# Optimization experiments

Measured on AMD Instinct MI355X. Metric: run time of the kernel, lower is better.

The kernel has to match this reference:

```python
import jax, jax.numpy as jnp
import numpy as np

STRIDE = (2, 2)
PADDING = (1, 1)
OUTPUT_PADDING = (0, 0)


def setup_inputs() -> dict:
    key = jax.random.key(0)
    k1, k2, k3 = jax.random.split(key, 3)
    B, Cin, H, W = 16, 32, 128, 128
    Cout, Kh, Kw = 32, 4, 4
    signal = jax.random.normal(k1, (B, Cin, H, W), dtype=jnp.float32)
    # conv_transpose weight layout: (Cin, Cout/groups, Kh, Kw)
    weight = jax.random.normal(k2, (Cin, Cout, Kh, Kw), dtype=jnp.float32) * 0.05
    bias = jax.random.normal(k3, (Cout,), dtype=jnp.float32)
    return {"signal": signal, "weight": weight, "bias": bias}


def reference(signal, weight, bias):
    """FFT-based 2D transposed convolution (stride 2, padding 1, groups=1, dilation=1).

    Matches torch.nn.functional.conv_transpose2d semantics:
      y[n] = sum_m x[m] * w[n - m*s], cropped by `padding` on each side.
    """
    sh, sw = STRIDE
    ph, pw = PADDING
    oph, opw = OUTPUT_PADDING
    B, Cin, H, W = signal.shape
    _, Cout, Kh, Kw = weight.shape

    # 1) zero-stuff the input by the stride (lhs dilation)
    Hu, Wu = (H - 1) * sh + 1, (W - 1) * sw + 1
    xu = jnp.zeros((B, Cin, Hu, Wu), dtype=signal.dtype)
    xu = xu.at[:, :, ::sh, ::sw].set(signal)

    # 2) full (true) convolution of upsampled signal with the weight via rFFT
    Nh, Nw = Hu + Kh - 1, Wu + Kw - 1  # full-conv output size == FFT size
    Xf = jnp.fft.rfft2(xu, s=(Nh, Nw))          # (B, Cin, Nh, Nw//2+1) complex64
    Wf = jnp.fft.rfft2(weight, s=(Nh, Nw))      # (Cin, Cout, Nh, Nw//2+1) complex64
    Yf = jnp.einsum('bihw,iohw->bohw', Xf, Wf)  # contract over input channels
    y = jnp.fft.irfft2(Yf, s=(Nh, Nw))          # (B, Cout, Nh, Nw) float32

    # 3) crop by padding; output_padding extends the end (zero here)
    out_h = (H - 1) * sh - 2 * ph + Kh + oph
    out_w = (W - 1) * sw - 2 * pw + Kw + opw
    y = y[:, :, ph:ph + out_h, pw:pw + out_w]

    # 4) bias
    return y + bias[None, :, None, None]
```

## Files before the change

kernel.cpp:

```cpp
#include <hip/hip_runtime.h>

#define B_    16
#define CIN   32
#define H_    128
#define W_    128
#define COUT  32
#define OH_   256
#define OW_   256
#define HP    130
#define WP    130

typedef __attribute__((ext_vector_type(8))) short bf8_t;
typedef __attribute__((ext_vector_type(4))) float f32x4;

__device__ inline unsigned short f2bf(float f) {
    unsigned int u = __float_as_uint(f);
    unsigned int r = (u + 0x7fffu + ((u >> 16) & 1u)) >> 16;
    return (unsigned short)r;
}

__global__ __launch_bounds__(256)
void prep_w(const float* __restrict__ wgt, unsigned short* __restrict__ wt) {
    for (int e = threadIdx.x; e < 16 * 32 * 32; e += 256) {
        int khkw = e >> 10;
        int co   = (e >> 5) & 31;
        int ci   = e & 31;
        wt[e] = f2bf(wgt[(ci * COUT + co) * 16 + khkw]);
    }
}

__global__ __launch_bounds__(256)
void prep_x(const float* __restrict__ x, unsigned short* __restrict__ xt) {
    const int n = blockIdx.y;
    const int h = blockIdx.x * 2 + (threadIdx.x >> 7);
    const int w = threadIdx.x & 127;
    const float* xp = x + (((long)n * CIN) * H_ + h) * W_ + w;
    unsigned short* op = xt + (((long)n * HP + (h + 1)) * WP + (w + 1)) * 32;
    const int sw = (w >> 1) & 3;
#pragma unroll
    for (int g = 0; g < 4; ++g) {
        union { unsigned short s[8]; uint4 q; } pk;
#pragma unroll
        for (int j = 0; j < 8; ++j)
            pk.s[j] = f2bf(xp[(long)(g * 8 + j) * (H_ * W_)]);
        *(uint4*)(op + (g ^ sw) * 8) = pk.q;
    }
}

__global__ __launch_bounds__(256)
void convt_mfma(const unsigned short* __restrict__ xt,
                const unsigned short* __restrict__ wt,
                const float* __restrict__ bias,
                float* __restrict__ y) {
    __shared__ unsigned short xs[4 * 66 * 32];

    const int tid  = threadIdx.x;
    const int lane = tid & 63;
    const int wv   = tid >> 6;
    const int n    = blockIdx.z;
    const int t0   = blockIdx.y * 2;
    const int u0   = blockIdx.x * 64;

    {
        const int r = wv;
        const unsigned short* gsrc = xt + (((long)n * HP + (t0 + r)) * WP + u0) * 32;
        unsigned short* lrow = xs + r * (66 * 32);
#pragma unroll
        for (int it = 0; it < 5; ++it) {
            int c = it * 64 + lane;
            if (c < 264) {
                __builtin_amdgcn_global_load_lds(
                    (const __attribute__((address_space(1))) void*)(gsrc + c * 8),
                    (__attribute__((address_space(3))) void*)(lrow + c * 8),
                    16, 0, 0);
            }
        }
    }

    const int ch   = wv & 1;
    const int trow = wv >> 1;
    const int g    = lane >> 4;
    const int li   = lane & 15;

    bf8_t wf[16];
    {
        const unsigned short* wp = wt + (ch * 16 + li) * 32 + g * 8;
#pragma unroll
        for (int kk = 0; kk < 16; ++kk)
            wf[kk] = *(const bf8_t*)(wp + kk * 1024);
    }
    float bias4[4];
#pragma unroll
    for (int r = 0; r < 4; ++r) bias4[r] = bias[ch * 16 + g * 4 + r];

    __syncthreads();

    const int t = t0 + trow;
#pragma unroll
    for (int st = 0; st < 4; ++st) {
        const int us = u0 + st * 16;

        bf8_t xf[3][3];
#pragma unroll
        for (int dh = 0; dh < 3; ++dh) {
#pragma unroll
            for (int dw = 0; dw < 3; ++dw) {
                int wg   = us + li + dw - 1;
                int wl   = wg - (u0 - 1);
                int slot = g ^ ((wg >> 1) & 3);
                int hl   = trow + dh;
                xf[dh][dw] = *(const bf8_t*)(xs + (hl * 66 + wl) * 32 + slot * 8);
            }
        }

        f32x4 acc[2][2];
#pragma unroll
        for (int po = 0; po < 2; ++po)
#pragma unroll
            for (int qo = 0; qo < 2; ++qo)
                acc[po][qo] = (f32x4){bias4[0], bias4[1], bias4[2], bias4[3]};

#pragma unroll
        for (int po = 0; po < 2; ++po) {
            const int dh0 = po ? 2 : 1, kh0 = po ? 0 : 1;
            const int dh1 = po ? 1 : 0, kh1 = po ? 2 : 3;
#pragma unroll
            for (int qo = 0; qo < 2; ++qo) {
                const int dw0 = qo ? 2 : 1, kw0 = qo ? 0 : 1;
                const int dw1 = qo ? 1 : 0, kw1 = qo ? 2 : 3;
                acc[po][qo] = __builtin_amdgcn_mfma_f32_16x16x32_bf16(
                    wf[kh0 * 4 + kw0], xf[dh0][dw0], acc[po][qo], 0, 0, 0);
                acc[po][qo] = __builtin_amdgcn_mfma_f32_16x16x32_bf16(
                    wf[kh0 * 4 + kw1], xf[dh0][dw1], acc[po][qo], 0, 0, 0);
                acc[po][qo] = __builtin_amdgcn_mfma_f32_16x16x32_bf16(
                    wf[kh1 * 4 + kw0], xf[dh1][dw0], acc[po][qo], 0, 0, 0);
                acc[po][qo] = __builtin_amdgcn_mfma_f32_16x16x32_bf16(
                    wf[kh1 * 4 + kw1], xf[dh1][dw1], acc[po][qo], 0, 0, 0);
            }
        }

#pragma unroll
        for (int po = 0; po < 2; ++po) {
            const int oh = 2 * t + po;
#pragma unroll
            for (int r = 0; r < 4; ++r) {
                const int co = ch * 16 + g * 4 + r;
                float* yp = y + (((long)(n * COUT + co) * OH_ + oh) * OW_) + 2 * (us + li);
                *(float2*)yp = make_float2(acc[po][0][r], acc[po][1][r]);
            }
        }
    }
}

extern "C" void kernel_launch(void* const* d_in, const int* in_sizes, int n_in,
                              void* d_out, int out_size, void* d_ws, size_t ws_size,
                              hipStream_t stream) {
    const float* x = (const float*)d_in[0];
    const float* w = (const float*)d_in[1];
    const float* b = (const float*)d_in[2];
    float* y = (float*)d_out;

    unsigned short* wt = (unsigned short*)d_ws;
    unsigned short* xt = (unsigned short*)((char*)d_ws + 32768);
    const size_t xt_bytes = (size_t)B_ * HP * WP * 32 * 2;

    hipMemsetAsync(xt, 0, xt_bytes, stream);
    prep_w<<<1, 256, 0, stream>>>(w, wt);
    prep_x<<<dim3(H_ / 2, B_), 256, 0, stream>>>(x, xt);
    convt_mfma<<<dim3(W_ / 64, H_ / 2, B_), 256, 0, stream>>>(xt, wt, b, y);
}
```

Before: 181.0 us.

## Fuse input bf16 conversion and padding into the MFMA transposed-conv kernel

Removes the separate memset and prep_x passes, which padded and converted the input to a bf16 channel-last buffer. The main kernel now reads fp32 input directly, converts it to bf16 and writes it swizzled into LDS, handling halo zeros with bounds checks. Blocks grow to 512 threads covering 4 output input-rows with a 6-row LDS tile. prep_w is also spread across 64 blocks. This saves a full round trip of the intermediate buffer and two launches, but the fused loads are strided fp32 channel reads and the halo rows are re-read by neighbouring blocks.

```diff
diff --git a/kernel.cpp b/kernel.cpp
--- a/kernel.cpp
+++ b/kernel.cpp
@@ -7,74 +7,75 @@
 #define COUT  32
 #define OH_   256
 #define OW_   256
-#define HP    130
-#define WP    130
 
 typedef __attribute__((ext_vector_type(8))) short bf8_t;
 typedef __attribute__((ext_vector_type(4))) float f32x4;
 
-__device__ inline unsigned short f2bf(float f) {
+__device__ inline unsigned int f2bf(float f) {
     unsigned int u = __float_as_uint(f);
-    unsigned int r = (u + 0x7fffu + ((u >> 16) & 1u)) >> 16;
-    return (unsigned short)r;
+    return (u + 0x7fffu + ((u >> 16) & 1u)) >> 16;
 }
 
 __global__ __launch_bounds__(256)
 void prep_w(const float* __restrict__ wgt, unsigned short* __restrict__ wt) {
-    for (int e = threadIdx.x; e < 16 * 32 * 32; e += 256) {
-        int khkw = e >> 10;
-        int co   = (e >> 5) & 31;
-        int ci   = e & 31;
-        wt[e] = f2bf(wgt[(ci * COUT + co) * 16 + khkw]);
-    }
+    int e = blockIdx.x * 256 + threadIdx.x;
+    int khkw = e >> 10, co = (e >> 5) & 31, ci = e & 31;
+    wt[e] = (unsigned short)f2bf(wgt[(ci * COUT + co) * 16 + khkw]);
 }
 
-__global__ __launch_bounds__(256)
-void prep_x(const float* __restrict__ x, unsigned short* __restrict__ xt) {
-    const int n = blockIdx.y;
-    const int h = blockIdx.x * 2 + (threadIdx.x >> 7);
-    const int w = threadIdx.x & 127;
-    const float* xp = x + (((long)n * CIN) * H_ + h) * W_ + w;
-    unsigned short* op = xt + (((long)n * HP + (h + 1)) * WP + (w + 1)) * 32;
-    const int sw = (w >> 1) & 3;
-#pragma unroll
-    for (int g = 0; g < 4; ++g) {
-        union { unsigned short s[8]; uint4 q; } pk;
-#pragma unroll
-        for (int j = 0; j < 8; ++j)
-            pk.s[j] = f2bf(xp[(long)(g * 8 + j) * (H_ * W_)]);
-        *(uint4*)(op + (g ^ sw) * 8) = pk.q;
-    }
-}
-
-__global__ __launch_bounds__(256)
-void convt_mfma(const unsigned short* __restrict__ xt,
-                const unsigned short* __restrict__ wt,
-                const float* __restrict__ bias,
-                float* __restrict__ y) {
-    __shared__ unsigned short xs[4 * 66 * 32];
+__global__ __launch_bounds__(512)
+void convt_fused(const float* __restrict__ x,
+                 const unsigned short* __restrict__ wt,
+                 const float* __restrict__ bias,
+                 float* __restrict__ y) {
+    __shared__ unsigned short xs[6 * 66 * 32];
 
     const int tid  = threadIdx.x;
     const int lane = tid & 63;
     const int wv   = tid >> 6;
     const int n    = blockIdx.z;
-    const int t0   = blockIdx.y * 2;
+    const int t0   = blockIdx.y * 4;
     const int u0   = blockIdx.x * 64;
 
-    {
-        const int r = wv;
-        const unsigned short* gsrc = xt + (((long)n * HP + (t0 + r)) * WP + u0) * 32;
-        unsigned short* lrow = xs + r * (66 * 32);
 #pragma unroll
-        for (int it = 0; it < 5; ++it) {
-            int c = it * 64 + lane;
-            if (c < 264) {
-                __builtin_amdgcn_global_load_lds(
-                    (const __attribute__((address_space(1))) void*)(gsrc + c * 8),
-                    (__attribute__((address_space(3))) void*)(lrow + c * 8),
-                    16, 0, 0);
-            }
-        }
+    for (int j = 0; j < 3; ++j) {
+        const int c  = wv + j * 8;
+        const int hr = c >> 2, gp = c & 3;
+        const int ih = t0 - 1 + hr;
+        const int iw = u0 - 1 + lane;
+        const bool inb = ((unsigned)ih < H_) && ((unsigned)iw < W_);
+        const float* xq = x + (((long)(n * CIN + gp * 8) * H_ + ih) * W_ + iw);
+        float v[8];
+#pragma unroll
+        for (int k = 0; k < 8; ++k)
+            v[k] = inb ? xq[(long)k * (H_ * W_)] : 0.0f;
+        uint4 pk;
+        pk.x = f2bf(v[0]) | (f2bf(v[1]) << 16);
+        pk.y = f2bf(v[2]) | (f2bf(v[3]) << 16);
+        pk.z = f2bf(v[4]) | (f2bf(v[5]) << 16);
+        pk.w = f2bf(v[6]) | (f2bf(v[7]) << 16);
+        const int slot = gp ^ ((iw >> 1) & 3);
+        *(uint4*)(xs + (hr * 66 + lane) * 32 + slot * 8) = pk;
+    }
+    if (tid < 48) {
+        const int c  = tid >> 1;
+        const int hr = c >> 2, gp = c & 3;
+        const int wc = 64 + (tid & 1);
+        const int ih = t0 - 1 + hr;
+        const int iw = u0 - 1 + wc;
+        const bool inb = ((unsigned)ih < H_) && ((unsigned)iw < W_);
+        const float* xq = x + (((long)(n * CIN + gp * 8) * H_ + ih) * W_ + iw);
+        float v[8];
+#pragma unroll
+        for (int k = 0; k < 8; ++k)
+            v[k] = inb ? xq[(long)k * (H_ * W_)] : 0.0f;
+        uint4 pk;
+        pk.x = f2bf(v[0]) | (f2bf(v[1]) << 16);
+        pk.y = f2bf(v[2]) | (f2bf(v[3]) << 16);
+        pk.z = f2bf(v[4]) | (f2bf(v[5]) << 16);
+        pk.w = f2bf(v[6]) | (f2bf(v[7]) << 16);
+        const int slot = gp ^ ((iw >> 1) & 3);
+        *(uint4*)(xs + (hr * 66 + wc) * 32 + slot * 8) = pk;
     }
 
     const int ch   = wv & 1;
@@ -161,11 +162,7 @@
     float* y = (float*)d_out;
 
     unsigned short* wt = (unsigned short*)d_ws;
-    unsigned short* xt = (unsigned short*)((char*)d_ws + 32768);
-    const size_t xt_bytes = (size_t)B_ * HP * WP * 32 * 2;
 
-    hipMemsetAsync(xt, 0, xt_bytes, stream);
-    prep_w<<<1, 256, 0, stream>>>(w, wt);
-    prep_x<<<dim3(H_ / 2, B_), 256, 0, stream>>>(x, xt);
-    convt_mfma<<<dim3(W_ / 64, H_ / 2, B_), 256, 0, stream>>>(xt, wt, b, y);
+    prep_w<<<64, 256, 0, stream>>>(w, wt);
+    convt_fused<<<dim3(W_ / 64, H_ / 4, B_), 512, 0, stream>>>(x, wt, b, y);
 }
```

Result: faster. 172.7 us (-4.6%).
